# Kernel tuning notes

Hardware: AMD Instinct MI355X
Metric: run time of the kernel (lower is better)

The kernel has to match this reference:

```python
import jax, jax.numpy as jnp
import numpy as np

NUM_SYMBOLS = 5
NUM_SUBCARRIERS = 33


def _dft_matrix(n):
    # Unitary DFT matrix: F[j,k] = exp(-2i*pi*j*k/n) / sqrt(n)
    omega = np.exp(-2j * np.pi / n)
    j, k = np.meshgrid(np.arange(n), np.arange(n))
    return (np.power(omega, j * k) / np.sqrt(n)).astype(np.complex64)


def setup_inputs() -> dict:
    key = jax.random.key(0)
    k1, k2 = jax.random.split(key)
    shape = (4096, NUM_SYMBOLS, 4, 4, NUM_SUBCARRIERS)  # (N, S, TXH, TXW, W)
    x_real = jax.random.normal(k1, shape, dtype=jnp.float32)
    x_imag = jax.random.normal(k2, shape, dtype=jnp.float32)
    F_sym = _dft_matrix(NUM_SYMBOLS)
    F_sub = _dft_matrix(NUM_SUBCARRIERS)
    return {
        "x_real": x_real,
        "x_imag": x_imag,
        "F_sym_real": jnp.asarray(F_sym.real, dtype=jnp.float32),
        "F_sym_imag": jnp.asarray(F_sym.imag, dtype=jnp.float32),
        "F_sub_real": jnp.asarray(F_sub.real, dtype=jnp.float32),
        "F_sub_imag": jnp.asarray(F_sub.imag, dtype=jnp.float32),
    }


def reference(x_real, x_imag, F_sym_real, F_sym_imag, F_sub_real, F_sub_imag):
    N, S, TXH, TXW, W = x_real.shape
    x = jax.lax.complex(x_real, x_imag).reshape(N, S, TXH * TXW, W)
    x = jnp.transpose(x, (0, 2, 1, 3))  # (N, A, S, W), A = TXH*TXW

    F_sym = jax.lax.complex(F_sym_real, F_sym_imag)  # (S, S)
    F_sub = jax.lax.complex(F_sub_real, F_sub_imag)  # (W, W)

    # 2D DFT across symbols (left) and subcarriers (right)
    X = jnp.einsum("st,natw->nasw", F_sym, x)
    X = jnp.einsum("nasw,wv->nasv", X, F_sub)

    # magnitude-square (power spectrum)
    X_mag_sq = (X.real * X.real + X.imag * X.imag).astype(jnp.complex64)

    # inverse 2D DFT (conjugate transposes) -> autocorrelation
    X = jnp.einsum("st,natw->nasw", F_sym.conj().T, X_mag_sq)
    X = jnp.einsum("nasw,wv->nasv", X, F_sub.conj().T)

    X = jnp.transpose(X, (0, 2, 1, 3))  # (N, S, A, W)
    return X.reshape(N, S, TXH, TXW, W)
```

## Files before the change

### kernel.cpp

```cpp
#include <hip/hip_runtime.h>

#define NS 5
#define NW 33
#define NA 16
#define SW 165
#define BUFS 99
#define MPW 5
#define GM 20
#define TPM 11
#define CPT 3
#define THREADS 256

#define CW0 19
#define CH0 (CW0*NS)
#define CE0 (CH0*MPW)
#define IT0 8
#define CW1 14
#define CH1 (CW1*NS)
#define CE1 (CH1*MPW)
#define IT1 6

typedef float f2 __attribute__((ext_vector_type(2)));

__device__ __forceinline__ void cmac(f2& z, f2 x, f2 f) {
    asm("v_pk_fma_f32 %0, %1, %2, %0 op_sel:[0,0,0] op_sel_hi:[1,0,1]"
        : "+v"(z) : "v"(x), "v"(f));
    asm("v_pk_fma_f32 %0, %1, %2, %0 op_sel:[1,1,0] op_sel_hi:[0,1,1] neg_lo:[1,0,0]"
        : "+v"(z) : "v"(x), "v"(f));
}

__device__ __forceinline__ void cmacr(f2& z, f2 f, f2 Pp) {
    asm("v_pk_fma_f32 %0, %1, %2, %0 op_sel:[0,0,0] op_sel_hi:[1,1,1] neg_hi:[1,0,0]"
        : "+v"(z) : "v"(f), "v"(Pp));
}

__device__ __forceinline__ void pkfma(f2& z, f2 a, f2 b) {
    asm("v_pk_fma_f32 %0, %1, %2, %0 op_sel:[0,0,0] op_sel_hi:[1,1,1]"
        : "+v"(z) : "v"(a), "v"(b));
}

#define STAGE(CW, CH, CE, NIT, W0)                                         \
    {                                                                      \
        f2 rr[NIT];                                                        \
        _Pragma("unroll")                                                  \
        for (int i = 0; i < NIT; ++i) {                                    \
            const int e = lane + i * 64;                                   \
            f2 v = (f2){0.f, 0.f};                                         \
            if (e < (CE)) {                                                \
                const int gq = e / (CH), rq = e - gq * (CH);               \
                const int tq = rq / (CW), wq = rq - tq * (CW);             \
                const int Mq = Mw + gq;                                    \
                if (Mq < NM) {                                             \
                    const int nq = Mq >> 4, aq = Mq & 15;                  \
                    const int go = ((nq * NS + tq) * NA + aq) * NW + (W0) + wq; \
                    v = (f2){x_real[go], x_imag[go]};                      \
                }                                                          \
            }                                                              \
            rr[i] = v;                                                     \
        }                                                                  \
        _Pragma("unroll")                                                  \
        for (int i = 0; i < NIT; ++i) {                                    \
            const int e = lane + i * 64;                                   \
            if (e < (CE)) {                                                \
                const int gq = e / (CH), rq = e - gq * (CH);               \
                const int tq = rq / (CW), wq = rq - tq * (CW);             \
                wbuf[gq * BUFS + wq * NS + tq] = rr[i];                    \
            }                                                              \
        }                                                                  \
    }

#define COMPUTE_CHUNK(CW, W0)                                              \
    if (act) {                                                             \
        const f2* bp = wbuf + gg * BUFS;                                   \
        _Pragma("unroll 3")                                                \
        for (int w = 0; w < (CW); ++w) {                                   \
            f2 xc[NS];                                                     \
            _Pragma("unroll")                                              \
            for (int t = 0; t < NS; ++t) xc[t] = bp[w * NS + t];           \
            f2 fv[CPT];                                                    \
            _Pragma("unroll")                                              \
            for (int k = 0; k < CPT; ++k)                                  \
                fv[k] = sFsub[((W0) + w) * NW + c0 + k];                   \
            _Pragma("unroll")                                              \
            for (int t = 0; t < NS; ++t)                                   \
                _Pragma("unroll")                                          \
                for (int k = 0; k < CPT; ++k)                              \
                    cmac(V[t][k], xc[t], fv[k]);                           \
        }                                                                  \
    }

__global__ __launch_bounds__(THREADS, 6) void autocorr_kernel(
    const float* __restrict__ x_real, const float* __restrict__ x_imag,
    const float* __restrict__ Fsym_re, const float* __restrict__ Fsym_im,
    const float* __restrict__ Fsub_re, const float* __restrict__ Fsub_im,
    float* __restrict__ out, int NM, int write_complex)
{
    __shared__ f2 sFsym[NS * NS];
    __shared__ f2 sFsub[NW * NW];
    __shared__ f2 buf[GM * BUFS];

    const int tid = threadIdx.x;
    const int wave = tid >> 6;
    const int lane = tid & 63;
    const int Mw = blockIdx.x * GM + wave * MPW;
    f2* const wbuf = &buf[wave * MPW * BUFS];

    for (int i = tid; i < NW * NW; i += THREADS)
        sFsub[i] = (f2){Fsub_re[i], Fsub_im[i]};
    if (tid < NS * NS) sFsym[tid] = (f2){Fsym_re[tid], Fsym_im[tid]};

    STAGE(CW0, CH0, CE0, IT0, 0);
    __syncthreads();

    const int g = lane / TPM;
    const int j = lane - g * TPM;
    const bool act = (lane < MPW * TPM);
    const int gg = act ? g : 0;
    const int M = Mw + gg;
    const int c0 = 3 * j;

    f2 V[NS][CPT];
#pragma unroll
    for (int t = 0; t < NS; ++t)
#pragma unroll
        for (int k = 0; k < CPT; ++k) V[t][k] = (f2){0.f, 0.f};

    COMPUTE_CHUNK(CW0, 0);

    STAGE(CW1, CH1, CE1, IT1, CW0);
    asm volatile("s_waitcnt lgkmcnt(0)" ::: "memory");

    COMPUTE_CHUNK(CW1, CW0);

    f2 T2[3][CPT];
#pragma unroll
    for (int p = 0; p < 3; ++p)
#pragma unroll
        for (int k = 0; k < CPT; ++k) T2[p][k] = (f2){0.f, 0.f};
    if (act) {
#pragma unroll
        for (int s = 0; s < NS; ++s) {
            f2 X[CPT];
#pragma unroll
            for (int k = 0; k < CPT; ++k) X[k] = (f2){0.f, 0.f};
#pragma unroll
            for (int t = 0; t < NS; ++t) {
                f2 f = sFsym[s * NS + t];
#pragma unroll
                for (int k = 0; k < CPT; ++k)
                    cmac(X[k], f, V[t][k]);
            }
#pragma unroll
            for (int k = 0; k < CPT; ++k) {
                const float Pv = X[k].x * X[k].x + X[k].y * X[k].y;
                const f2 Pp = (f2){Pv, Pv};
#pragma unroll
                for (int p = 0; p < 3; ++p)
                    cmacr(T2[p][k], sFsym[s * NS + p], Pp);
            }
        }
        f2* const wb = wbuf + gg * BUFS;
#pragma unroll
        for (int k = 0; k < CPT; ++k)
#pragma unroll
            for (int p = 0; p < 3; ++p)
                wb[(c0 + k) * 3 + p] = T2[p][k];
    }
    asm volatile("s_waitcnt lgkmcnt(0)" ::: "memory");

    if (act) {
        const f2* bp = wbuf + gg * BUFS;
        if (!write_complex) {
            f2 Ypk[3][CPT];
#pragma unroll
            for (int p = 0; p < 3; ++p)
#pragma unroll
                for (int k = 0; k < CPT; ++k) Ypk[p][k] = (f2){0.f, 0.f};
#pragma unroll 3
            for (int v = 0; v < NW; ++v) {
                f2 tc[3];
#pragma unroll
                for (int p = 0; p < 3; ++p) tc[p] = bp[v * 3 + p];
                f2 fw[CPT];
#pragma unroll
                for (int k = 0; k < CPT; ++k) fw[k] = sFsub[(c0 + k) * NW + v];
#pragma unroll
                for (int p = 0; p < 3; ++p)
#pragma unroll
                    for (int k = 0; k < CPT; ++k)
                        pkfma(Ypk[p][k], tc[p], fw[k]);
            }
            if (M < NM) {
                const int n = M >> 4, a = M & 15;
                const int obase = ((n * NS) * NA + a) * NW;
#pragma unroll
                for (int p = 0; p < 3; ++p) {
                    const int pp = (NS - p) % NS;
#pragma unroll
                    for (int k = 0; k < CPT; ++k) {
                        const int q = c0 + k;
                        const int qq = (NW - q) % NW;
                        const float Yr = Ypk[p][k].x + Ypk[p][k].y;
                        out[obase + p * (NA * NW) + q] = Yr;
                        out[obase + pp * (NA * NW) + qq] = Yr;
                    }
                }
            }
        } else {
            f2 Y[3][CPT];
#pragma unroll
            for (int p = 0; p < 3; ++p)
#pragma unroll
                for (int k = 0; k < CPT; ++k) Y[p][k] = (f2){0.f, 0.f};
            for (int v = 0; v < NW; ++v) {
                f2 tc[3];
#pragma unroll
                for (int p = 0; p < 3; ++p) tc[p] = bp[v * 3 + p];
                f2 fw[CPT];
#pragma unroll
                for (int k = 0; k < CPT; ++k) fw[k] = sFsub[(c0 + k) * NW + v];
#pragma unroll
                for (int p = 0; p < 3; ++p)
#pragma unroll
                    for (int k = 0; k < CPT; ++k) {
                        Y[p][k].x = fmaf(tc[p].x, fw[k].x, Y[p][k].x);
                        Y[p][k].x = fmaf(tc[p].y, fw[k].y, Y[p][k].x);
                        Y[p][k].y = fmaf(tc[p].y, fw[k].x, Y[p][k].y);
                        Y[p][k].y = fmaf(-tc[p].x, fw[k].y, Y[p][k].y);
                    }
            }
            if (M < NM) {
                const int n = M >> 4, a = M & 15;
#pragma unroll
                for (int p = 0; p < 3; ++p) {
                    const int pp = (NS - p) % NS;
#pragma unroll
                    for (int k = 0; k < CPT; ++k) {
                        const int q = c0 + k;
                        const int qq = (NW - q) % NW;
                        ((float2*)out)[((n * NS + p) * NA + a) * NW + q] =
                            make_float2(Y[p][k].x, Y[p][k].y);
                        ((float2*)out)[((n * NS + pp) * NA + a) * NW + qq] =
                            make_float2(Y[p][k].x, -Y[p][k].y);
                    }
                }
            }
        }
    }
}

extern "C" void kernel_launch(void* const* d_in, const int* in_sizes, int n_in,
                              void* d_out, int out_size, void* d_ws, size_t ws_size,
                              hipStream_t stream) {
    const float* x_real  = (const float*)d_in[0];
    const float* x_imag  = (const float*)d_in[1];
    const float* Fsym_re = (const float*)d_in[2];
    const float* Fsym_im = (const float*)d_in[3];
    const float* Fsub_re = (const float*)d_in[4];
    const float* Fsub_im = (const float*)d_in[5];

    const int NM = in_sizes[0] / SW;
    const long long n_cplx = (long long)in_sizes[0];
    const int write_complex = ((long long)out_size >= 2 * n_cplx) ? 1 : 0;

    const int blocks = (NM + GM - 1) / GM;

    autocorr_kernel<<<blocks, THREADS, 0, stream>>>(
        x_real, x_imag, Fsym_re, Fsym_im, Fsub_re, Fsub_im,
        (float*)d_out, NM, write_complex);
}
```

Before: 179.6 us.

## Exploit DFT conjugate symmetry to halve subcarrier and symbol transform FMAs

Rewrites the forward subcarrier DFT to pair columns w and 33-w, forming sums and differences so each Fsub value multiplies both at once. The symbol DFT gets the same pairing over t and 5-t, and the inverse subcarrier pass pairs v and 33-v. Staging now splits the data by symbol instead of by subcarrier chunk, and LDS addresses are precomputed. This cuts the complex multiply-accumulate count by about half, at the cost of extra add/sub instructions and a correctness dependence on the F matrices being exactly symmetric DFT matrices.

```diff
diff --git a/kernel.cpp b/kernel.cpp
--- a/kernel.cpp
+++ b/kernel.cpp
@@ -11,81 +11,114 @@
 #define CPT 3
 #define THREADS 256
 
-#define CW0 19
-#define CH0 (CW0*NS)
-#define CE0 (CH0*MPW)
+#define C0T 3
+#define C0E (C0T*NW*MPW)
 #define IT0 8
-#define CW1 14
-#define CH1 (CW1*NS)
-#define CE1 (CH1*MPW)
+#define C1T 2
+#define C1E (C1T*NW*MPW)
 #define IT1 6
 
 typedef float f2 __attribute__((ext_vector_type(2)));
 
-__device__ __forceinline__ void cmac(f2& z, f2 x, f2 f) {
+__device__ __forceinline__ void cmac_re(f2& z, f2 u, f2 f) {
     asm("v_pk_fma_f32 %0, %1, %2, %0 op_sel:[0,0,0] op_sel_hi:[1,0,1]"
-        : "+v"(z) : "v"(x), "v"(f));
+        : "+v"(z) : "v"(u), "v"(f));
+}
+__device__ __forceinline__ void cmac_im(f2& z, f2 d, f2 f) {
     asm("v_pk_fma_f32 %0, %1, %2, %0 op_sel:[1,1,0] op_sel_hi:[0,1,1] neg_lo:[1,0,0]"
-        : "+v"(z) : "v"(x), "v"(f));
-}
-
+        : "+v"(z) : "v"(d), "v"(f));
+}
 __device__ __forceinline__ void cmacr(f2& z, f2 f, f2 Pp) {
     asm("v_pk_fma_f32 %0, %1, %2, %0 op_sel:[0,0,0] op_sel_hi:[1,1,1] neg_hi:[1,0,0]"
         : "+v"(z) : "v"(f), "v"(Pp));
 }
-
 __device__ __forceinline__ void pkfma(f2& z, f2 a, f2 b) {
     asm("v_pk_fma_f32 %0, %1, %2, %0 op_sel:[0,0,0] op_sel_hi:[1,1,1]"
         : "+v"(z) : "v"(a), "v"(b));
 }
-
-#define STAGE(CW, CH, CE, NIT, W0)                                         \
+__device__ __forceinline__ f2 pkadd(f2 a, f2 b) {
+    f2 r; asm("v_pk_add_f32 %0, %1, %2" : "=v"(r) : "v"(a), "v"(b)); return r;
+}
+__device__ __forceinline__ f2 pksub(f2 a, f2 b) {
+    f2 r; asm("v_pk_add_f32 %0, %1, %2 neg_lo:[0,1] neg_hi:[0,1]"
+              : "=v"(r) : "v"(a), "v"(b)); return r;
+}
+__device__ __forceinline__ f2 pkaddsub(f2 a, f2 b) {
+    f2 r; asm("v_pk_add_f32 %0, %1, %2 neg_hi:[0,1]"
+              : "=v"(r) : "v"(a), "v"(b)); return r;
+}
+__device__ __forceinline__ f2 pkmul_re(f2 u, f2 f) {
+    f2 r; asm("v_pk_mul_f32 %0, %1, %2 op_sel:[0,0] op_sel_hi:[1,0]"
+              : "=v"(r) : "v"(u), "v"(f)); return r;
+}
+__device__ __forceinline__ f2 pkmul(f2 a, f2 b) {
+    f2 r; asm("v_pk_mul_f32 %0, %1, %2" : "=v"(r) : "v"(a), "v"(b)); return r;
+}
+
+#define STAGE(NT, CE_, NIT, T0)                                            \
     {                                                                      \
-        f2 rr[NIT];                                                        \
+        f2 rr[NIT]; int dsa[NIT];                                          \
         _Pragma("unroll")                                                  \
         for (int i = 0; i < NIT; ++i) {                                    \
             const int e = lane + i * 64;                                   \
             f2 v = (f2){0.f, 0.f};                                         \
-            if (e < (CE)) {                                                \
-                const int gq = e / (CH), rq = e - gq * (CH);               \
-                const int tq = rq / (CW), wq = rq - tq * (CW);             \
+            int da = 0;                                                    \
+            if (e < (CE_)) {                                               \
+                const int gq = e / ((NT) * NW), rq = e - gq * ((NT) * NW); \
+                const int tq = rq / NW, wq = rq - tq * NW;                 \
                 const int Mq = Mw + gq;                                    \
+                da = gq * BUFS + wq * (NT) + tq;                           \
                 if (Mq < NM) {                                             \
                     const int nq = Mq >> 4, aq = Mq & 15;                  \
-                    const int go = ((nq * NS + tq) * NA + aq) * NW + (W0) + wq; \
+                    const int go = (nq * NS + (T0) + tq) * (NA * NW) + aq * NW + wq; \
                     v = (f2){x_real[go], x_imag[go]};                      \
                 }                                                          \
             }                                                              \
-            rr[i] = v;                                                     \
+            rr[i] = v; dsa[i] = da;                                        \
         }                                                                  \
         _Pragma("unroll")                                                  \
         for (int i = 0; i < NIT; ++i) {                                    \
             const int e = lane + i * 64;                                   \
-            if (e < (CE)) {                                                \
-                const int gq = e / (CH), rq = e - gq * (CH);               \
-                const int tq = rq / (CW), wq = rq - tq * (CW);             \
-                wbuf[gq * BUFS + wq * NS + tq] = rr[i];                    \
+            if (e < (CE_)) wbuf[dsa[i]] = rr[i];                           \
+        }                                                                  \
+    }
+
+#define COMPUTE_CHUNK(NT, TBASE)                                           \
+    if (act) {                                                             \
+        const f2* bp = wbuf + gg * BUFS;                                   \
+        {                                               \
+            f2 fv[CPT];                                                    \
+            _Pragma("unroll")                                              \
+            for (int k = 0; k < CPT; ++k) fv[k] = sFsub[c0 + k];           \
+            _Pragma("unroll")                                              \
+            for (int t = 0; t < (NT); ++t) {                               \
+                const f2 xc = bp[t];                                       \
+                _Pragma("unroll")                                          \
+                for (int k = 0; k < CPT; ++k)                              \
+                    V[(TBASE) + t][k] = pkmul_re(xc, fv[k]);               \
             }                                                              \
         }                                                                  \
-    }
-
-#define COMPUTE_CHUNK(CW, W0)                                              \
-    if (act) {                                                             \
-        const f2* bp = wbuf + gg * BUFS;                                   \
-        _Pragma("unroll 3")                                                \
-        for (int w = 0; w < (CW); ++w) {                                   \
-            f2 xc[NS];                                                     \
-            _Pragma("unroll")                                              \
-            for (int t = 0; t < NS; ++t) xc[t] = bp[w * NS + t];           \
+        _Pragma("unroll 4")                                                \
+        for (int wp = 1; wp <= 16; ++wp) {                                 \
+            const int wq = NW - wp;                                        \
+            f2 xcA[NT], xcB[NT];                                           \
+            _Pragma("unroll")                                              \
+            for (int t = 0; t < (NT); ++t) xcA[t] = bp[wp * (NT) + t];     \
+            _Pragma("unroll")                                              \
+            for (int t = 0; t < (NT); ++t) xcB[t] = bp[wq * (NT) + t];     \
             f2 fv[CPT];                                                    \
             _Pragma("unroll")                                              \
-            for (int k = 0; k < CPT; ++k)                                  \
-                fv[k] = sFsub[((W0) + w) * NW + c0 + k];                   \
-            _Pragma("unroll")                                              \
-            for (int t = 0; t < NS; ++t)                                   \
+            for (int k = 0; k < CPT; ++k) fv[k] = sFsub[wp * NW + c0 + k]; \
+            _Pragma("unroll")                                              \
+            for (int t = 0; t < (NT); ++t) {                               \
+                const f2 u = pkadd(xcA[t], xcB[t]);                        \
+                const f2 d = pksub(xcA[t], xcB[t]);                        \
                 _Pragma("unroll")                                          \
-                for (int k = 0; k < CPT; ++k)                              \
-                    cmac(V[t][k], xc[t], fv[k]);                           \
+                for (int k = 0; k < CPT; ++k) {                            \
+                    cmac_re(V[(TBASE) + t][k], u, fv[k]);                  \
+                    cmac_im(V[(TBASE) + t][k], d, fv[k]);                  \
+                }                                                          \
+            }                                                              \
         }                                                                  \
     }
 
@@ -109,7 +142,7 @@
         sFsub[i] = (f2){Fsub_re[i], Fsub_im[i]};
     if (tid < NS * NS) sFsym[tid] = (f2){Fsym_re[tid], Fsym_im[tid]};
 
-    STAGE(CW0, CH0, CE0, IT0, 0);
+    STAGE(C0T, C0E, IT0, 0);
     __syncthreads();
 
     const int g = lane / TPM;
@@ -120,17 +153,13 @@
     const int c0 = 3 * j;
 
     f2 V[NS][CPT];
-#pragma unroll
-    for (int t = 0; t < NS; ++t)
-#pragma unroll
-        for (int k = 0; k < CPT; ++k) V[t][k] = (f2){0.f, 0.f};
-
-    COMPUTE_CHUNK(CW0, 0);
-
-    STAGE(CW1, CH1, CE1, IT1, CW0);
+
+    COMPUTE_CHUNK(C0T, 0);
+
+    STAGE(C1T, C1E, IT1, C0T);
     asm volatile("s_waitcnt lgkmcnt(0)" ::: "memory");
 
-    COMPUTE_CHUNK(CW1, CW0);
+    COMPUTE_CHUNK(C1T, C0T);
 
     f2 T2[3][CPT];
 #pragma unroll
@@ -139,16 +168,23 @@
         for (int k = 0; k < CPT; ++k) T2[p][k] = (f2){0.f, 0.f};
     if (act) {
 #pragma unroll
+        for (int k = 0; k < CPT; ++k) {
+            f2 a = V[1][k], b = V[4][k];
+            V[1][k] = pkadd(a, b); V[4][k] = pksub(a, b);
+            a = V[2][k]; b = V[3][k];
+            V[2][k] = pkadd(a, b); V[3][k] = pksub(a, b);
+        }
+#pragma unroll
         for (int s = 0; s < NS; ++s) {
+            const f2 f0 = sFsym[s * NS + 0];
+            const f2 f1 = sFsym[s * NS + 1];
+            const f2 fc2 = sFsym[s * NS + 2];
             f2 X[CPT];
 #pragma unroll
-            for (int k = 0; k < CPT; ++k) X[k] = (f2){0.f, 0.f};
-#pragma unroll
-            for (int t = 0; t < NS; ++t) {
-                f2 f = sFsym[s * NS + t];
-#pragma unroll
-                for (int k = 0; k < CPT; ++k)
-                    cmac(X[k], f, V[t][k]);
+            for (int k = 0; k < CPT; ++k) {
+                X[k] = pkmul_re(V[0][k], f0);
+                cmac_re(X[k], V[1][k], f1); cmac_im(X[k], V[4][k], f1);
+                cmac_re(X[k], V[2][k], fc2); cmac_im(X[k], V[3][k], fc2);
             }
 #pragma unroll
             for (int k = 0; k < CPT; ++k) {
@@ -172,23 +208,37 @@
         const f2* bp = wbuf + gg * BUFS;
         if (!write_complex) {
             f2 Ypk[3][CPT];
-#pragma unroll
-            for (int p = 0; p < 3; ++p)
-#pragma unroll
-                for (int k = 0; k < CPT; ++k) Ypk[p][k] = (f2){0.f, 0.f};
-#pragma unroll 3
-            for (int v = 0; v < NW; ++v) {
-                f2 tc[3];
-#pragma unroll
-                for (int p = 0; p < 3; ++p) tc[p] = bp[v * 3 + p];
+            {
                 f2 fw[CPT];
 #pragma unroll
-                for (int k = 0; k < CPT; ++k) fw[k] = sFsub[(c0 + k) * NW + v];
+                for (int k = 0; k < CPT; ++k) fw[k] = sFsub[(c0 + k) * NW];
+#pragma unroll
+                for (int p = 0; p < 3; ++p) {
+                    const f2 tc = bp[p];
+#pragma unroll
+                    for (int k = 0; k < CPT; ++k)
+                        Ypk[p][k] = pkmul(tc, fw[k]);
+                }
+            }
+#pragma unroll 4
+            for (int vp = 1; vp <= 16; ++vp) {
+                const int vq = NW - vp;
+                f2 tcA[3], tcB[3];
+#pragma unroll
+                for (int p = 0; p < 3; ++p) tcA[p] = bp[vp * 3 + p];
+#pragma unroll
+                for (int p = 0; p < 3; ++p) tcB[p] = bp[vq * 3 + p];
+                f2 e2[3];
+#pragma unroll
+                for (int p = 0; p < 3; ++p) e2[p] = pkaddsub(tcA[p], tcB[p]);
+                f2 fw[CPT];
+#pragma unroll
+                for (int k = 0; k < CPT; ++k) fw[k] = sFsub[(c0 + k) * NW + vp];
 #pragma unroll
                 for (int p = 0; p < 3; ++p)
 #pragma unroll
                     for (int k = 0; k < CPT; ++k)
-                        pkfma(Ypk[p][k], tc[p], fw[k]);
+                        pkfma(Ypk[p][k], e2[p], fw[k]);
             }
             if (M < NM) {
                 const int n = M >> 4, a = M & 15;
```

Result: faster. 175.6 us (-2.2%).
